# Kernel optimization log

Measured on AMD Instinct MI355X. Metric: run time of the kernel, lower is better.

Reference implementation:

```python
import jax, jax.numpy as jnp
import numpy as np

N_NODES = 100000
N_EDGES = 1600000
C_IN, C_HID, C_OUT = 128, 128, 64


def setup_inputs() -> dict:
    key = jax.random.key(0)
    k1, k2, k3, k4, k5, k6 = jax.random.split(key, 6)
    x = jax.random.normal(k1, (N_NODES, C_IN), dtype=jnp.float32)
    edge_index = jax.random.randint(k2, (2, N_EDGES), 0, N_NODES, dtype=jnp.int64)
    # Glorot-style init for GCN weights, zero bias (PyG defaults)
    W1 = jax.random.normal(k3, (C_IN, C_HID), dtype=jnp.float32) * (1.0 / np.sqrt(C_IN))
    b1 = jnp.zeros((C_HID,), dtype=jnp.float32)
    W2 = jax.random.normal(k4, (C_HID, C_OUT), dtype=jnp.float32) * (1.0 / np.sqrt(C_HID))
    b2 = jnp.zeros((C_OUT,), dtype=jnp.float32)
    return {"x": x, "edge_index": edge_index, "W1": W1, "b1": b1, "W2": W2, "b2": b2}


def _gcn_conv(x, W, b, src, dst, norm, n_nodes):
    # x' = D^-1/2 (A + I) D^-1/2 (x W) + b   (PyG GCNConv default)
    h = x @ W                                  # [N, out]
    msg = h[src] * norm[:, None]               # gather + scale, [E', out]
    out = jax.ops.segment_sum(msg, dst, num_segments=n_nodes)  # scatter-add
    return out + b


def reference(x, edge_index, W1, b1, W2, b2):
    n = x.shape[0]
    loops = jnp.arange(n, dtype=edge_index.dtype)
    src = jnp.concatenate([edge_index[0], loops])  # self-loops appended
    dst = jnp.concatenate([edge_index[1], loops])
    # symmetric normalization: deg from destination index (incl. self-loops)
    deg = jax.ops.segment_sum(jnp.ones_like(dst, dtype=x.dtype), dst, num_segments=n)
    dis = jnp.where(deg > 0, jax.lax.rsqrt(deg), 0.0)
    norm = dis[src] * dis[dst]                 # [E + N]
    h = _gcn_conv(x, W1, b1, src, dst, norm, n)
    h = jax.nn.relu(h)                          # Dropout is identity at inference
    out = _gcn_conv(h, W2, b2, src, dst, norm, n)
    return out
```

## Files before the change

### kernel.cpp

```cpp
#include <hip/hip_runtime.h>

static constexpr int NPAD = 131072;
static constexpr int PAD = 48;
typedef unsigned int uint32;

__device__ __forceinline__ ushort f2bf(float f) {
  uint32 u = __float_as_uint(f);
  return (ushort)((u + 0x7FFF + ((u >> 16) & 1)) >> 16);
}
__device__ __forceinline__ float bf_lo(uint32 u) { return __uint_as_float(u << 16); }
__device__ __forceinline__ float bf_hi(uint32 u) { return __uint_as_float(u & 0xFFFF0000u); }

__device__ __forceinline__ int lane_rank_in(unsigned long long mask) {
  return __builtin_amdgcn_mbcnt_hi((unsigned int)(mask >> 32),
                                   __builtin_amdgcn_mbcnt_lo((unsigned int)mask, 0));
}

__device__ __forceinline__ void bucket_body(const int* __restrict__ src,
                                            const int* __restrict__ dst,
                                            int* __restrict__ bcur,
                                            uint2* __restrict__ buckets,
                                            int* __restrict__ degi, int nN, int nE,
                                            unsigned long long magic, int bcap,
                                            int bb) {
  __shared__ int cnt[8];
  __shared__ int blkbase[8];
  const int t = threadIdx.x;
  {
    int z = bb * 256 + t;
    if (z < nN) degi[z] = 0;
  }
  if (t < 8) cnt[t] = 0;
  __syncthreads();
  const int e0 = bb * 2048;
  int sa[8], da[8], ba[8], off[8];
  bool va[8];
#pragma unroll
  for (int p = 0; p < 2; ++p) {
    int idx = e0 + p * 1024 + t * 4;
    if (idx + 4 <= nE) {
      int4 sv = *(const int4*)(src + idx);
      int4 dv = *(const int4*)(dst + idx);
      sa[p * 4 + 0] = sv.x; sa[p * 4 + 1] = sv.y; sa[p * 4 + 2] = sv.z; sa[p * 4 + 3] = sv.w;
      da[p * 4 + 0] = dv.x; da[p * 4 + 1] = dv.y; da[p * 4 + 2] = dv.z; da[p * 4 + 3] = dv.w;
      va[p * 4 + 0] = va[p * 4 + 1] = va[p * 4 + 2] = va[p * 4 + 3] = true;
    } else {
#pragma unroll
      for (int j = 0; j < 4; ++j) {
        int ii = idx + j;
        bool v = ii < nE;
        va[p * 4 + j] = v;
        sa[p * 4 + j] = v ? src[ii] : 0;
        da[p * 4 + j] = v ? dst[ii] : 0;
      }
    }
  }
#pragma unroll
  for (int j = 0; j < 8; ++j) {
    ba[j] = (int)(((unsigned long long)(uint32)da[j] * magic) >> 35);
    unsigned long long mv = __ballot(va[j]);
    unsigned long long m0 = __ballot((ba[j] & 1) != 0);
    unsigned long long m1 = __ballot((ba[j] & 2) != 0);
    unsigned long long m2 = __ballot((ba[j] & 4) != 0);
    unsigned long long meq = ((ba[j] & 1) ? m0 : ~m0) & ((ba[j] & 2) ? m1 : ~m1) &
                             ((ba[j] & 4) ? m2 : ~m2) & mv;
    if (va[j]) {
      int rank = lane_rank_in(meq);
      int tot = __popcll(meq);
      int leader = __ffsll(meq) - 1;
      int base = 0;
      if (rank == 0) base = atomicAdd(&cnt[ba[j]], tot);
      base = __shfl(base, leader, 64);
      off[j] = base + rank;
    } else {
      off[j] = 0;
    }
  }
  __syncthreads();
  if (t < 8) blkbase[t] = t * bcap + atomicAdd(&bcur[t], cnt[t]);
  __syncthreads();
#pragma unroll
  for (int j = 0; j < 8; ++j) {
    if (va[j]) buckets[blkbase[ba[j]] + off[j]] = make_uint2((uint32)sa[j], (uint32)da[j]);
  }
}

template <int COLS, bool RELU_IN>
__device__ __forceinline__ void gemm_body(const float* __restrict__ X,
                                          const float* __restrict__ W,
                                          ushort* __restrict__ H, int n, int bid) {
  constexpr int KC = 32;
  constexpr int RT = 132;
  constexpr int TN = (COLS == 128) ? 8 : 4;
  __shared__ float sX[KC][RT];
  __shared__ float sW[KC][COLS];
  const int t = threadIdx.x;
  const int row0 = bid * 128;
  const int r0 = (t >> 4) * 8;
  const int c0 = (t & 15) * 4;

  float acc[8][TN];
#pragma unroll
  for (int i = 0; i < 8; ++i)
#pragma unroll
    for (int j = 0; j < TN; ++j) acc[i][j] = 0.f;

  for (int k0 = 0; k0 < 128; k0 += KC) {
#pragma unroll
    for (int p = 0; p < 4; ++p) {
      int idx = p * 256 + t;
      int r = idx >> 3;
      int f = idx & 7;
      int gr = row0 + r;
      float4 v = make_float4(0.f, 0.f, 0.f, 0.f);
      if (gr < n) v = *(const float4*)(X + (size_t)gr * 128 + k0 + f * 4);
      if (RELU_IN) {
        v.x = fmaxf(v.x, 0.f); v.y = fmaxf(v.y, 0.f);
        v.z = fmaxf(v.z, 0.f); v.w = fmaxf(v.w, 0.f);
      }
      int kk = f * 4;
      sX[kk + 0][r] = v.x; sX[kk + 1][r] = v.y;
      sX[kk + 2][r] = v.z; sX[kk + 3][r] = v.w;
    }
    constexpr int WP = (KC * COLS) / (256 * 4);
#pragma unroll
    for (int p = 0; p < WP; ++p) {
      int idx = p * 256 + t;
      int k = idx / (COLS / 4);
      int c4 = idx % (COLS / 4);
      *(float4*)&sW[k][c4 * 4] = *(const float4*)(W + (size_t)(k0 + k) * COLS + c4 * 4);
    }
    __syncthreads();
#pragma unroll 8
    for (int k = 0; k < KC; ++k) {
      float4 xa = *(const float4*)&sX[k][r0];
      float4 xb = *(const float4*)&sX[k][r0 + 4];
      float4 wa = *(const float4*)&sW[k][c0];
      float xr[8] = {xa.x, xa.y, xa.z, xa.w, xb.x, xb.y, xb.z, xb.w};
      if (COLS == 128) {
        float4 wb = *(const float4*)&sW[k][c0 + 64];
        float wr[8] = {wa.x, wa.y, wa.z, wa.w, wb.x, wb.y, wb.z, wb.w};
#pragma unroll
        for (int i = 0; i < 8; ++i)
#pragma unroll
          for (int j = 0; j < 8; ++j) acc[i][j] = fmaf(xr[i], wr[j], acc[i][j]);
      } else {
        float wr[4] = {wa.x, wa.y, wa.z, wa.w};
#pragma unroll
        for (int i = 0; i < 8; ++i)
#pragma unroll
          for (int j = 0; j < 4; ++j) acc[i][j] = fmaf(xr[i], wr[j], acc[i][j]);
      }
    }
    __syncthreads();
  }
#pragma unroll
  for (int i = 0; i < 8; ++i) {
    int row = row0 + r0 + i;
    if (row >= n) break;
    ushort* hrow = H + (size_t)row * COLS;
    ushort4 s0;
    s0.x = f2bf(acc[i][0]); s0.y = f2bf(acc[i][1]);
    s0.z = f2bf(acc[i][2]); s0.w = f2bf(acc[i][3]);
    *(ushort4*)&hrow[c0] = s0;
    if (COLS == 128) {
      ushort4 s1;
      s1.x = f2bf(acc[i][4]); s1.y = f2bf(acc[i][5]);
      s1.z = f2bf(acc[i][6]); s1.w = f2bf(acc[i][7]);
      *(ushort4*)&hrow[c0 + 64] = s1;
    }
  }
}

__global__ __launch_bounds__(256) void gemm1_bucket_kernel(
    const float* __restrict__ X, const float* __restrict__ W,
    ushort* __restrict__ H, int n, const int* __restrict__ src,
    const int* __restrict__ dst, int* __restrict__ bcur,
    uint2* __restrict__ buckets, int* __restrict__ degi, int nE,
    unsigned long long magic, int bcap, int gemmBlocks) {
  const int b = (int)blockIdx.x;
  if (b < gemmBlocks) {
    gemm_body<128, false>(X, W, H, n, b);
  } else {
    bucket_body(src, dst, bcur, buckets, degi, n, nE, magic, bcap, b - gemmBlocks);
  }
}

__global__ __launch_bounds__(256) void gemm2_kernel(const float* __restrict__ X,
                                                    const float* __restrict__ W,
                                                    ushort* __restrict__ H, int n) {
  gemm_body<64, true>(X, W, H, n, (int)blockIdx.x);
}

__global__ __launch_bounds__(256) void fillpad_kernel(const uint2* __restrict__ buckets,
                                                      const int* __restrict__ bcur,
                                                      int* __restrict__ degi,
                                                      int* __restrict__ csrp, int bcap) {
  const int xcd = blockIdx.x & 7;
  const int sub = blockIdx.x >> 3;
  const int nsub = gridDim.x >> 3;
  const int cntb = bcur[xcd];
  const uint2* B = buckets + (size_t)xcd * bcap;
  for (int i = sub * 256 + threadIdx.x; i < cntb; i += nsub * 256) {
    uint2 e = B[i];
    int pos = atomicAdd(&degi[(int)e.y], 1);
    if (pos < PAD) csrp[(size_t)e.y * PAD + pos] = (int)e.x;
  }
}

template <int COLS>
__global__ __launch_bounds__(256) void agg_kernel(const int* __restrict__ degi,
                                                  const int* __restrict__ csrp,
                                                  const ushort* __restrict__ h,
                                                  const float* __restrict__ bias,
                                                  float* __restrict__ out, int n,
                                                  int nPerXcd) {
  __shared__ uint2 sE[4][64];
  const int t = threadIdx.x;
  const int lane = t & 63;
  const int wid = t >> 6;
  const int xcd = blockIdx.x & 7;
  const int sub = (int)blockIdx.x >> 3;
  const int nwv = (gridDim.x >> 3) * 4;
  const int d0 = xcd * nPerXcd;
  const int d1 = min(d0 + nPerXcd, n);
  float2 bv2 = make_float2(0.f, 0.f);
  float bv1 = 0.f;
  if (COLS == 128) bv2 = ((const float2*)bias)[lane];
  else bv1 = bias[lane];

  int d = d0 + sub * 4 + wid;
  if (d >= d1) return;

  int degA = min(degi[d], PAD);
  int sA = (lane < degA) ? csrp[(size_t)d * PAD + lane] : 0;
  float wA = (lane < degA) ? rsqrtf((float)degi[sA] + 1.0f) : 0.f;
  int dB = d + nwv;
  int degB = 0, sRawB = 0;
  if (dB < d1) {
    degB = degi[dB];
    if (lane < PAD) sRawB = csrp[(size_t)dB * PAD + lane];
  }

  while (true) {
    const float dd = rsqrtf((float)degA + 1.0f);
    const bool hasB = dB < d1;
    int sB = 0, gB = 0;
    if (hasB) {
      int dgc = min(degB, PAD);
      sB = (lane < dgc) ? sRawB : 0;
      gB = degi[sB];
    }
    const int dC = dB + nwv;
    int degC = 0, sRawC = 0;
    if (dC < d1) {
      degC = degi[dC];
      if (lane < PAD) sRawC = csrp[(size_t)dC * PAD + lane];
    }
    sE[wid][lane] = make_uint2((uint32)sA, __float_as_uint(wA));
    if (COLS == 128) {
      uint32 hv = ((const uint32*)(h + (size_t)d * 128))[lane];
      float acx = 0.f, acy = 0.f;
      for (int j0 = 0; j0 < degA; j0 += 8) {
        uint32 a[8];
        float w[8];
#pragma unroll
        for (int k = 0; k < 8; ++k) {
          uint2 e = sE[wid][j0 + k];
          w[k] = __uint_as_float(e.y);
          a[k] = ((const uint32*)(h + (size_t)e.x * 128))[lane];
        }
#pragma unroll
        for (int k = 0; k < 8; ++k) {
          acx = fmaf(w[k], bf_lo(a[k]), acx);
          acy = fmaf(w[k], bf_hi(a[k]), acy);
        }
      }
      float ox = fmaf(dd, fmaf(dd, bf_lo(hv), acx), bv2.x);
      float oy = fmaf(dd, fmaf(dd, bf_hi(hv), acy), bv2.y);
      ((float2*)(out + (size_t)d * 128))[lane] = make_float2(ox, oy);
    } else {
      uint32 hv = (uint32)h[(size_t)d * 64 + lane];
      float acc = 0.f;
      for (int j0 = 0; j0 < degA; j0 += 8) {
        uint32 a[8];
        float w[8];
#pragma unroll
        for (int k = 0; k < 8; ++k) {
          uint2 e = sE[wid][j0 + k];
          w[k] = __uint_as_float(e.y);
          a[k] = (uint32)h[(size_t)e.x * 64 + lane];
        }
#pragma unroll
        for (int k = 0; k < 8; ++k) acc = fmaf(w[k], bf_lo(a[k]), acc);
      }
      out[(size_t)d * 64 + lane] = fmaf(dd, fmaf(dd, bf_lo(hv), acc), bv1);
    }
    if (!hasB) break;
    const int dgc = min(degB, PAD);
    wA = (lane < dgc) ? rsqrtf((float)gB + 1.0f) : 0.f;
    sA = sB;
    degA = dgc;
    d = dB;
    dB = dC;
    degB = degC;
    sRawB = sRawC;
  }
}

extern "C" void kernel_launch(void* const* d_in, const int* in_sizes, int n_in,
                              void* d_out, int out_size, void* d_ws, size_t ws_size,
                              hipStream_t stream) {
  const float* x  = (const float*)d_in[0];
  const int* ei   = (const int*)d_in[1];
  const float* W1 = (const float*)d_in[2];
  const float* b1 = (const float*)d_in[3];
  const float* W2 = (const float*)d_in[4];
  const float* b2 = (const float*)d_in[5];
  float* out = (float*)d_out;

  const int N = in_sizes[0] / 128;
  const int E = in_sizes[1] / 2;
  const int* srcI = ei;
  const int* dstI = ei + E;
  const int nPerXcd = (N + 7) / 8;
  const unsigned long long magic =
      ((1ULL << 35) + (unsigned long long)nPerXcd - 1) / (unsigned long long)nPerXcd;

  char* w = (char*)d_ws;
  int* degi       = (int*)w;                   w += (size_t)NPAD * 4;
  int* bcur       = (int*)w;                   w += 64 * 4;
  int* csrp       = (int*)w;                   w += (size_t)(N + 64) * PAD * 4;
  ushort* h       = (ushort*)w;                w += (size_t)N * 128 * 2;
  float* out1     = (float*)w;
  ushort* g       = h;
  uint2* buckets  = (uint2*)out1;
  const int bcap = E / 8 + 16384;

  const int gemmBlocks = (N + 127) / 128;
  const int bucketBlocks = (E + 2047) / 2048;

  hipMemsetAsync(bcur, 0, 64 * sizeof(int), stream);
  gemm1_bucket_kernel<<<gemmBlocks + bucketBlocks, 256, 0, stream>>>(
      x, W1, h, N, srcI, dstI, bcur, buckets, degi, E, magic, bcap, gemmBlocks);
  fillpad_kernel<<<2048, 256, 0, stream>>>(buckets, bcur, degi, csrp, bcap);
  agg_kernel<128><<<2048, 256, 0, stream>>>(degi, csrp, h, b1, out1, N, nPerXcd);
  gemm2_kernel<<<gemmBlocks, 256, 0, stream>>>(out1, W2, g, N);
  agg_kernel<64><<<2048, 256, 0, stream>>>(degi, csrp, g, b2, out, N, nPerXcd);
}
```

Measured before the change: 348.9 us.

## Use split-fp16 MFMA for dense transforms in both GCN layers

Replaces the scalar FP32 register-tiled GEMM with an MFMA 16x16x32 f16 path. Each fp32 operand is split into a high and a low fp16 part, and three products are accumulated to keep near-fp32 accuracy. The aim is to cut the ALU cost of the X·W transforms, which share a launch with edge bucketing. In exchange it adds conversion work, strided transposed LDS writes for W, and scalar 2-byte output stores.

```diff
diff --git a/kernel.cpp b/kernel.cpp
--- a/kernel.cpp
+++ b/kernel.cpp
@@ -3,6 +3,10 @@
 static constexpr int NPAD = 131072;
 static constexpr int PAD = 48;
 typedef unsigned int uint32;
+typedef _Float16 f16;
+typedef __attribute__((ext_vector_type(8))) _Float16 f16x8;
+typedef __attribute__((ext_vector_type(4))) _Float16 f16x4;
+typedef __attribute__((ext_vector_type(4))) float f32x4;
 
 __device__ __forceinline__ ushort f2bf(float f) {
   uint32 u = __float_as_uint(f);
@@ -86,26 +90,30 @@
 }
 
 template <int COLS, bool RELU_IN>
-__device__ __forceinline__ void gemm_body(const float* __restrict__ X,
-                                          const float* __restrict__ W,
-                                          ushort* __restrict__ H, int n, int bid) {
-  constexpr int KC = 32;
-  constexpr int RT = 132;
-  constexpr int TN = (COLS == 128) ? 8 : 4;
-  __shared__ float sX[KC][RT];
-  __shared__ float sW[KC][COLS];
+__device__ __forceinline__ void gemm_mfma_body(const float* __restrict__ X,
+                                               const float* __restrict__ W,
+                                               ushort* __restrict__ H, int n,
+                                               int bid) {
+  constexpr int NS = COLS / 16;
+  constexpr int LDK = 40;
+  __shared__ f16 sAh[128][LDK];
+  __shared__ f16 sAl[128][LDK];
+  __shared__ f16 sBh[COLS][LDK];
+  __shared__ f16 sBl[COLS][LDK];
   const int t = threadIdx.x;
   const int row0 = bid * 128;
-  const int r0 = (t >> 4) * 8;
-  const int c0 = (t & 15) * 4;
-
-  float acc[8][TN];
-#pragma unroll
-  for (int i = 0; i < 8; ++i)
-#pragma unroll
-    for (int j = 0; j < TN; ++j) acc[i][j] = 0.f;
-
-  for (int k0 = 0; k0 < 128; k0 += KC) {
+  const int wv = t >> 6;
+  const int l = t & 63;
+  const int fr = l & 15;
+  const int fkb = (l >> 4) * 8;
+
+  f32x4 acc[2][NS];
+#pragma unroll
+  for (int m = 0; m < 2; ++m)
+#pragma unroll
+    for (int nt = 0; nt < NS; ++nt) acc[m][nt] = (f32x4){0.f, 0.f, 0.f, 0.f};
+
+  for (int k0 = 0; k0 < 128; k0 += 32) {
 #pragma unroll
     for (int p = 0; p < 4; ++p) {
       int idx = p * 256 + t;
@@ -118,58 +126,54 @@
         v.x = fmaxf(v.x, 0.f); v.y = fmaxf(v.y, 0.f);
         v.z = fmaxf(v.z, 0.f); v.w = fmaxf(v.w, 0.f);
       }
-      int kk = f * 4;
-      sX[kk + 0][r] = v.x; sX[kk + 1][r] = v.y;
-      sX[kk + 2][r] = v.z; sX[kk + 3][r] = v.w;
-    }
-    constexpr int WP = (KC * COLS) / (256 * 4);
+      f16x4 hv, lv;
+      hv.x = (f16)v.x; lv.x = (f16)(v.x - (float)hv.x);
+      hv.y = (f16)v.y; lv.y = (f16)(v.y - (float)hv.y);
+      hv.z = (f16)v.z; lv.z = (f16)(v.z - (float)hv.z);
+      hv.w = (f16)v.w; lv.w = (f16)(v.w - (float)hv.w);
+      *(f16x4*)&sAh[r][f * 4] = hv;
+      *(f16x4*)&sAl[r][f * 4] = lv;
+    }
+    constexpr int WP = (32 * COLS) / (256 * 4);
 #pragma unroll
     for (int p = 0; p < WP; ++p) {
       int idx = p * 256 + t;
       int k = idx / (COLS / 4);
       int c4 = idx % (COLS / 4);
-      *(float4*)&sW[k][c4 * 4] = *(const float4*)(W + (size_t)(k0 + k) * COLS + c4 * 4);
+      float4 v = *(const float4*)(W + (size_t)(k0 + k) * COLS + c4 * 4);
+      f16 hh;
+      hh = (f16)v.x; sBh[c4 * 4 + 0][k] = hh; sBl[c4 * 4 + 0][k] = (f16)(v.x - (float)hh);
+      hh = (f16)v.y; sBh[c4 * 4 + 1][k] = hh; sBl[c4 * 4 + 1][k] = (f16)(v.y - (float)hh);
+      hh = (f16)v.z; sBh[c4 * 4 + 2][k] = hh; sBl[c4 * 4 + 2][k] = (f16)(v.z - (float)hh);
+      hh = (f16)v.w; sBh[c4 * 4 + 3][k] = hh; sBl[c4 * 4 + 3][k] = (f16)(v.w - (float)hh);
     }
     __syncthreads();
-#pragma unroll 8
-    for (int k = 0; k < KC; ++k) {
-      float4 xa = *(const float4*)&sX[k][r0];
-      float4 xb = *(const float4*)&sX[k][r0 + 4];
-      float4 wa = *(const float4*)&sW[k][c0];
-      float xr[8] = {xa.x, xa.y, xa.z, xa.w, xb.x, xb.y, xb.z, xb.w};
-      if (COLS == 128) {
-        float4 wb = *(const float4*)&sW[k][c0 + 64];
-        float wr[8] = {wa.x, wa.y, wa.z, wa.w, wb.x, wb.y, wb.z, wb.w};
-#pragma unroll
-        for (int i = 0; i < 8; ++i)
-#pragma unroll
-          for (int j = 0; j < 8; ++j) acc[i][j] = fmaf(xr[i], wr[j], acc[i][j]);
-      } else {
-        float wr[4] = {wa.x, wa.y, wa.z, wa.w};
-#pragma unroll
-        for (int i = 0; i < 8; ++i)
-#pragma unroll
-          for (int j = 0; j < 4; ++j) acc[i][j] = fmaf(xr[i], wr[j], acc[i][j]);
-      }
+    const f16x8 ah0 = *(const f16x8*)&sAh[wv * 32 + fr][fkb];
+    const f16x8 ah1 = *(const f16x8*)&sAh[wv * 32 + 16 + fr][fkb];
+    const f16x8 al0 = *(const f16x8*)&sAl[wv * 32 + fr][fkb];
+    const f16x8 al1 = *(const f16x8*)&sAl[wv * 32 + 16 + fr][fkb];
+#pragma unroll
+    for (int nt = 0; nt < NS; ++nt) {
+      const f16x8 bh = *(const f16x8*)&sBh[nt * 16 + fr][fkb];
+      const f16x8 bl = *(const f16x8*)&sBl[nt * 16 + fr][fkb];
+      acc[0][nt] = __builtin_amdgcn_mfma_f32_16x16x32_f16(ah0, bh, acc[0][nt], 0, 0, 0);
+      acc[1][nt] = __builtin_amdgcn_mfma_f32_16x16x32_f16(ah1, bh, acc[1][nt], 0, 0, 0);
+      acc[0][nt] = __builtin_amdgcn_mfma_f32_16x16x32_f16(al0, bh, acc[0][nt], 0, 0, 0);
+      acc[1][nt] = __builtin_amdgcn_mfma_f32_16x16x32_f16(al1, bh, acc[1][nt], 0, 0, 0);
+      acc[0][nt] = __builtin_amdgcn_mfma_f32_16x16x32_f16(ah0, bl, acc[0][nt], 0, 0, 0);
+      acc[1][nt] = __builtin_amdgcn_mfma_f32_16x16x32_f16(ah1, bl, acc[1][nt], 0, 0, 0);
     }
     __syncthreads();
   }
 #pragma unroll
-  for (int i = 0; i < 8; ++i) {
-    int row = row0 + r0 + i;
-    if (row >= n) break;
-    ushort* hrow = H + (size_t)row * COLS;
-    ushort4 s0;
-    s0.x = f2bf(acc[i][0]); s0.y = f2bf(acc[i][1]);
-    s0.z = f2bf(acc[i][2]); s0.w = f2bf(acc[i][3]);
-    *(ushort4*)&hrow[c0] = s0;
-    if (COLS == 128) {
-      ushort4 s1;
-      s1.x = f2bf(acc[i][4]); s1.y = f2bf(acc[i][5]);
-      s1.z = f2bf(acc[i][6]); s1.w = f2bf(acc[i][7]);
-      *(ushort4*)&hrow[c0 + 64] = s1;
-    }
-  }
+  for (int m = 0; m < 2; ++m)
+#pragma unroll
+    for (int nt = 0; nt < NS; ++nt)
+#pragma unroll
+      for (int j = 0; j < 4; ++j) {
+        int row = row0 + wv * 32 + m * 16 + (l >> 4) * 4 + j;
+        if (row < n) H[(size_t)row * COLS + nt * 16 + fr] = f2bf(acc[m][nt][j]);
+      }
 }
 
 __global__ __launch_bounds__(256) void gemm1_bucket_kernel(
@@ -180,7 +184,7 @@
     unsigned long long magic, int bcap, int gemmBlocks) {
   const int b = (int)blockIdx.x;
   if (b < gemmBlocks) {
-    gemm_body<128, false>(X, W, H, n, b);
+    gemm_mfma_body<128, false>(X, W, H, n, b);
   } else {
     bucket_body(src, dst, bcur, buckets, degi, n, nE, magic, bcap, b - gemmBlocks);
   }
@@ -189,7 +193,7 @@
 __global__ __launch_bounds__(256) void gemm2_kernel(const float* __restrict__ X,
                                                     const float* __restrict__ W,
                                                     ushort* __restrict__ H, int n) {
-  gemm_body<64, true>(X, W, H, n, (int)blockIdx.x);
+  gemm_mfma_body<64, true>(X, W, H, n, (int)blockIdx.x);
 }
 
 __global__ __launch_bounds__(256) void fillpad_kernel(const uint2* __restrict__ buckets,
```

New measurement: 334.6 us. -4.1%, faster.
